# Performance work log

Hardware: AMD Instinct MI355X
Metric: run time of the kernel (lower is better)

## Reference

```python
import jax, jax.numpy as jnp
import numpy as np

EPS = 1e-12

def _l2norm(v, axis):
    n = jnp.sqrt(jnp.sum(v * v, axis=axis, keepdims=True))
    return v / jnp.maximum(n, EPS)

def setup_inputs() -> dict:
    key = jax.random.key(0)
    k1, k2, k3, k4 = jax.random.split(key, 4)
    N, T, D, K = 8, 2048, 512, 64
    x = jax.random.normal(k1, (N, T, D), dtype=jnp.float32)
    W = jax.random.normal(k2, (K, D), dtype=jnp.float32) * (1.0 / np.sqrt(D))  # Conv1d(k=1) weight squeezed
    b = jax.random.normal(k3, (K,), dtype=jnp.float32) * 0.01
    centroids = jax.random.uniform(k4, (K, D), dtype=jnp.float32)
    return {"x": x, "W": W, "b": b, "centroids": centroids}

def reference(x, W, b, centroids):
    N, T, D = x.shape
    K = centroids.shape[0]
    # L2-normalize descriptors along feature dim
    xn = _l2norm(x, axis=2)                                  # [N,T,D]
    # Conv1d with kernel_size=1 == per-timestep linear: [N,K,T] logits over clusters
    logits = jnp.einsum('ntd,kd->nkt', xn, W) + b[None, :, None]
    a = jax.nn.softmax(logits, axis=1)                       # soft assignment over K
    # Algebraically equal to sum_t a[n,k,t] * (xn[n,t,:] - c[k,:])
    vlad = jnp.einsum('nkt,ntd->nkd', a, xn) \
         - jnp.sum(a, axis=2)[:, :, None] * centroids[None]  # [N,K,D]
    vlad = _l2norm(vlad, axis=2)                             # intra-normalize per cluster
    vlad = vlad.reshape(N, K * D)
    return _l2norm(vlad, axis=1)                             # global L2 normalize
```

## Files before the change

### kernel.cpp

```cpp
#include <hip/hip_runtime.h>
#include <math.h>

#define EPS 1e-12f
#define NN 8
#define TT 2048
#define DD 512
#define KK 64

typedef short short8 __attribute__((ext_vector_type(8)));
typedef float floatx4 __attribute__((ext_vector_type(4)));

__device__ __forceinline__ unsigned short f2bf(float f) {
    unsigned int u = __float_as_uint(f);
    u += 0x7FFFu + ((u >> 16) & 1u);
    return (unsigned short)(u >> 16);
}
__device__ __forceinline__ unsigned int pack2(float a, float b) {
    return (unsigned int)f2bf(a) | ((unsigned int)f2bf(b) << 16);
}


__global__ __launch_bounds__(256) void k0_prep(const float* __restrict__ W,
                                               unsigned short* __restrict__ Wb,
                                               float* __restrict__ asum) {
    int i = blockIdx.x * 256 + threadIdx.x;
    Wb[i] = f2bf(W[i]);
    if (i < NN * KK) asum[i] = 0.0f;
}

__global__ __launch_bounds__(256) void kA(const float* __restrict__ x,
                                          const unsigned short* __restrict__ Wb,
                                          const float* __restrict__ bias,
                                          unsigned short* __restrict__ xb,
                                          unsigned short* __restrict__ aTs,
                                          float* __restrict__ asum) {
    const int tid = threadIdx.x;
    const int w = tid >> 6, lane = tid & 63;
    const int l = lane & 15, q = lane >> 4;
    const int row0 = blockIdx.x * 64 + w * 16;
    const int row = row0 + l;
    const int n = row0 >> 11;
    const int tl0 = row0 & (TT - 1);

    const float* xr = x + (size_t)row * DD;
    unsigned short* xo = xb + (size_t)row * DD;
    short8 fragA[16];
    float ssq = 0.0f;
#pragma unroll
    for (int s = 0; s < 16; ++s) {
        float4 u0 = *(const float4*)(xr + s * 32 + q * 8);
        float4 u1 = *(const float4*)(xr + s * 32 + q * 8 + 4);
        ssq += u0.x*u0.x + u0.y*u0.y + u0.z*u0.z + u0.w*u0.w
             + u1.x*u1.x + u1.y*u1.y + u1.z*u1.z + u1.w*u1.w;
        uint4 pk;
        pk.x = pack2(u0.x, u0.y); pk.y = pack2(u0.z, u0.w);
        pk.z = pack2(u1.x, u1.y); pk.w = pack2(u1.z, u1.w);
        union { uint4 u; short8 s8; } cvt; cvt.u = pk;
        fragA[s] = cvt.s8;
        *(uint4*)(xo + s * 32 + q * 8) = pk;
    }
    ssq += __shfl_xor(ssq, 16, 64);
    ssq += __shfl_xor(ssq, 32, 64);
    float st = 1.0f / fmaxf(sqrtf(ssq), EPS);

    floatx4 acc[4];
#pragma unroll
    for (int h = 0; h < 4; ++h) acc[h] = floatx4{0.f, 0.f, 0.f, 0.f};
#pragma unroll
    for (int s = 0; s < 16; ++s) {
#pragma unroll
        for (int h = 0; h < 4; ++h) {
            short8 wf = *(const short8*)(Wb + (size_t)(h * 16 + l) * DD + s * 32 + q * 8);
            acc[h] = __builtin_amdgcn_mfma_f32_16x16x32_bf16(fragA[s], wf, acc[h], 0, 0, 0);
        }
    }

    float sr[4];
#pragma unroll
    for (int r = 0; r < 4; ++r) sr[r] = __shfl(st, 4 * q + r, 64);
    float bj[4];
#pragma unroll
    for (int h = 0; h < 4; ++h) bj[h] = bias[h * 16 + l];

    float av[4][4];
#pragma unroll
    for (int r = 0; r < 4; ++r) {
        float v0 = acc[0][r] * sr[r] + bj[0], v1 = acc[1][r] * sr[r] + bj[1];
        float v2 = acc[2][r] * sr[r] + bj[2], v3 = acc[3][r] * sr[r] + bj[3];
        float m = fmaxf(fmaxf(v0, v1), fmaxf(v2, v3));
#pragma unroll
        for (int msk = 1; msk <= 8; msk <<= 1) m = fmaxf(m, __shfl_xor(m, msk, 64));
        float e0 = __expf(v0 - m), e1 = __expf(v1 - m), e2 = __expf(v2 - m), e3 = __expf(v3 - m);
        float ssum = e0 + e1 + e2 + e3;
#pragma unroll
        for (int msk = 1; msk <= 8; msk <<= 1) ssum += __shfl_xor(ssum, msk, 64);
        float inv = 1.0f / ssum;
        av[0][r] = e0 * inv; av[1][r] = e1 * inv; av[2][r] = e2 * inv; av[3][r] = e3 * inv;
    }

#pragma unroll
    for (int h = 0; h < 4; ++h) {
        uint2 p;
        p.x = pack2(av[h][0] * sr[0], av[h][1] * sr[1]);
        p.y = pack2(av[h][2] * sr[2], av[h][3] * sr[3]);
        *(uint2*)(aTs + ((size_t)(n * KK + h * 16 + l)) * TT + tl0 + 4 * q) = p;
    }
#pragma unroll
    for (int h = 0; h < 4; ++h) {
        float sh = av[h][0] + av[h][1] + av[h][2] + av[h][3];
        sh += __shfl_xor(sh, 16, 64);
        sh += __shfl_xor(sh, 32, 64);
        if (q == 0) atomicAdd(&asum[n * KK + h * 16 + l], sh);
    }
}

__global__ __launch_bounds__(256) void kB(const unsigned short* __restrict__ xb,
                                          const unsigned short* __restrict__ aTs,
                                          float* __restrict__ part) {
    __shared__ unsigned char smem[17408];
    unsigned short* sX0 = (unsigned short*)smem;
    unsigned short* sX1 = sX0 + 4096;
    float* sT = (float*)smem;

    const int tid = threadIdx.x;
    const int wv = tid >> 6, lane = tid & 63;
    const int l = lane & 15, q = lane >> 4;
    const int bid = blockIdx.x;
    const int tc = bid & 7, dt = (bid >> 3) & 7, n = bid >> 6;

    const int ts = tid & 63, dq = tid >> 6;
    const unsigned short* xbase = xb + ((size_t)(n * TT + tc * 256)) * DD + dt * 64 + dq * 16;
    const int g = ts >> 3, t7 = ts & 7;

#define STAGE(S, BUF)                                                          \
    {                                                                          \
        const unsigned short* p_ = xbase + (size_t)((S) * 64 + ts) * DD;       \
        unsigned short vals[16];                                               \
        *(uint4*)(vals) = *(const uint4*)(p_);                                 \
        *(uint4*)(vals + 8) = *(const uint4*)(p_ + 8);                         \
        _Pragma("unroll")                                                      \
        for (int e = 0; e < 16; ++e) {                                         \
            int d_ = dq * 16 + e;                                              \
            (BUF)[d_ * 64 + ((g ^ (d_ & 7)) << 3) + t7] = vals[e];             \
        }                                                                      \
    }

    floatx4 acc[4];
#pragma unroll
    for (int nt = 0; nt < 4; ++nt) acc[nt] = floatx4{0.f, 0.f, 0.f, 0.f};
    const unsigned short* abase = aTs + ((size_t)(n * KK + wv * 16 + l)) * TT + tc * 256;

    STAGE(0, sX0);
    __syncthreads();
#pragma unroll
    for (int s = 0; s < 4; ++s) {
        unsigned short* cur = (s & 1) ? sX1 : sX0;
        unsigned short* nxt = (s & 1) ? sX0 : sX1;
        if (s < 3) {
            if (s == 0) STAGE(1, nxt)
            else if (s == 1) STAGE(2, nxt)
            else STAGE(3, nxt)
        }
#pragma unroll
        for (int kb = 0; kb < 2; ++kb) {
            short8 af = *(const short8*)(abase + s * 64 + kb * 32 + q * 8);
            int gg = q + 4 * kb;
#pragma unroll
            for (int nt = 0; nt < 4; ++nt) {
                int d = nt * 16 + l;
                short8 bf = *(const short8*)(cur + d * 64 + ((gg ^ (d & 7)) << 3));
                acc[nt] = __builtin_amdgcn_mfma_f32_16x16x32_bf16(af, bf, acc[nt], 0, 0, 0);
            }
        }
        __syncthreads();
    }
#undef STAGE

#pragma unroll
    for (int nt = 0; nt < 4; ++nt)
#pragma unroll
        for (int r = 0; r < 4; ++r)
            sT[(wv * 16 + 4 * q + r) * 68 + nt * 16 + l] = acc[nt][r];
    __syncthreads();

    float* pbase = part + ((size_t)(tc * 512 + n * KK)) * DD + dt * 64;
    const int fq = tid & 15, kr = tid >> 4;
#pragma unroll
    for (int i = 0; i < 4; ++i) {
        int k = i * 16 + kr;
        float4 val = *(float4*)(sT + k * 68 + fq * 4);
        *(float4*)(pbase + (size_t)k * DD + fq * 4) = val;
    }
}

__global__ __launch_bounds__(128) void kC(const float* __restrict__ part,
                                          const float* __restrict__ asum,
                                          const float* __restrict__ cent,
                                          float* __restrict__ v,
                                          float* __restrict__ norms) {
    __shared__ float red[2];
    const int nk = blockIdx.x;
    const int k = nk & 63;
    const int tid = threadIdx.x;
    float as = asum[nk];
    float4 cc = ((const float4*)(cent + (size_t)k * DD))[tid];
    float4 a4 = make_float4(-as * cc.x, -as * cc.y, -as * cc.z, -as * cc.w);
#pragma unroll
    for (int tc = 0; tc < 8; ++tc) {
        float4 p = ((const float4*)(part + ((size_t)(tc * 512 + nk)) * DD))[tid];
        a4.x += p.x; a4.y += p.y; a4.z += p.z; a4.w += p.w;
    }
    ((float4*)(v + (size_t)nk * DD))[tid] = a4;
    float ssq = a4.x*a4.x + a4.y*a4.y + a4.z*a4.z + a4.w*a4.w;
#pragma unroll
    for (int m = 32; m >= 1; m >>= 1) ssq += __shfl_xor(ssq, m, 64);
    if ((tid & 63) == 0) red[tid >> 6] = ssq;
    __syncthreads();
    if (tid == 0) norms[nk] = red[0] + red[1];
}

__global__ __launch_bounds__(256) void kD(const float* __restrict__ v,
                                          const float* __restrict__ norms,
                                          float* __restrict__ out) {
    const int n = blockIdx.x >> 3, kg = blockIdx.x & 7;
    const int tid = threadIdx.x;
    float g2 = 0.0f;
#pragma unroll
    for (int k = 0; k < 64; ++k) {
        float nr = sqrtf(norms[n * KK + k]);
        float t = nr / fmaxf(nr, EPS);
        g2 += t * t;
    }
    float g = sqrtf(g2);
    int k = kg * 8 + (tid >> 5);
    float nr = sqrtf(norms[n * KK + k]);
    float s = 1.0f / (fmaxf(nr, EPS) * fmaxf(g, EPS));
    const float4* vp = (const float4*)(v + ((size_t)(n * KK + k)) * DD) + (tid & 31) * 4;
    float4* op = (float4*)(out + ((size_t)(n * KK + k)) * DD) + (tid & 31) * 4;
#pragma unroll
    for (int i = 0; i < 4; ++i) {
        float4 t4 = vp[i];
        t4.x *= s; t4.y *= s; t4.z *= s; t4.w *= s;
        op[i] = t4;
    }
}

extern "C" void kernel_launch(void* const* d_in, const int* in_sizes, int n_in,
                              void* d_out, int out_size, void* d_ws, size_t ws_size,
                              hipStream_t stream) {
    const float* x    = (const float*)d_in[0];
    const float* W    = (const float*)d_in[1];
    const float* b    = (const float*)d_in[2];
    const float* cent = (const float*)d_in[3];
    float* out = (float*)d_out;

    float* w = (float*)d_ws;
    unsigned short* Wb  = (unsigned short*)(w + 0);
    unsigned short* xb  = (unsigned short*)(w + 16384);
    unsigned short* aTs = (unsigned short*)(w + 4210688);
    float* part  = w + 4734976;
    float* v     = w + 6832128;
    float* asum  = w + 7094272;
    float* norms = w + 7094784;

    hipLaunchKernelGGL(k0_prep, dim3(128), dim3(256), 0, stream, W, Wb, asum);
    hipLaunchKernelGGL(kA,      dim3(256), dim3(256), 0, stream, x, Wb, b, xb, aTs, asum);
    hipLaunchKernelGGL(kB,      dim3(512), dim3(256), 0, stream, xb, aTs, part);
    hipLaunchKernelGGL(kC,      dim3(512), dim3(128), 0, stream, part, asum, cent, v, norms);
    hipLaunchKernelGGL(kD,      dim3(64),  dim3(256), 0, stream, v, norms, out);
}
```

Before: 108.5 us.

## Fuse weight prep and final normalization, replace asum atomics with partials

Drops the separate W-to-bf16 prep kernel: each kA block converts W into a 64KB LDS tile laid out in MFMA fragment order. The asum atomics become per-block partial sums that kC reduces. kD is folded into kC, because after intra-normalization every cluster row has unit norm, so the global norm is the constant 8. It also remaps kB block indices. This cuts two launches and the intermediate v/norms traffic, but each kA block now re-reads all of W and uses a large LDS footprint.

```diff
diff --git a/kernel.cpp b/kernel.cpp
--- a/kernel.cpp
+++ b/kernel.cpp
@@ -20,21 +20,17 @@
 }
 
 
-__global__ __launch_bounds__(256) void k0_prep(const float* __restrict__ W,
-                                               unsigned short* __restrict__ Wb,
-                                               float* __restrict__ asum) {
-    int i = blockIdx.x * 256 + threadIdx.x;
-    Wb[i] = f2bf(W[i]);
-    if (i < NN * KK) asum[i] = 0.0f;
-}
-
 __global__ __launch_bounds__(256) void kA(const float* __restrict__ x,
-                                          const unsigned short* __restrict__ Wb,
+                                          const float* __restrict__ W,
                                           const float* __restrict__ bias,
                                           unsigned short* __restrict__ xb,
                                           unsigned short* __restrict__ aTs,
-                                          float* __restrict__ asum) {
+                                          float* __restrict__ asumP) {
+    __shared__ unsigned short sW[32768];
+    __shared__ float sRed[256];
+
     const int tid = threadIdx.x;
+
     const int w = tid >> 6, lane = tid & 63;
     const int l = lane & 15, q = lane >> 4;
     const int row0 = blockIdx.x * 64 + w * 16;
@@ -59,10 +55,28 @@
         fragA[s] = cvt.s8;
         *(uint4*)(xo + s * 32 + q * 8) = pk;
     }
+
+    {
+        const int sp = tid >> 4, hp = (tid >> 2) & 3, qp = tid & 3;
+        const float* wsrc = W + (size_t)(hp * 16) * DD + sp * 32 + qp * 8;
+        unsigned short* wdst = sW + (size_t)tid * 128;
+#pragma unroll
+        for (int j = 0; j < 16; ++j) {
+            float4 u0 = *(const float4*)(wsrc + (size_t)j * DD);
+            float4 u1 = *(const float4*)(wsrc + (size_t)j * DD + 4);
+            uint4 pk;
+            pk.x = pack2(u0.x, u0.y); pk.y = pack2(u0.z, u0.w);
+            pk.z = pack2(u1.x, u1.y); pk.w = pack2(u1.z, u1.w);
+            *(uint4*)(wdst + j * 8) = pk;
+        }
+    }
+
     ssq += __shfl_xor(ssq, 16, 64);
     ssq += __shfl_xor(ssq, 32, 64);
     float st = 1.0f / fmaxf(sqrtf(ssq), EPS);
 
+    __syncthreads();
+
     floatx4 acc[4];
 #pragma unroll
     for (int h = 0; h < 4; ++h) acc[h] = floatx4{0.f, 0.f, 0.f, 0.f};
@@ -70,7 +84,7 @@
     for (int s = 0; s < 16; ++s) {
 #pragma unroll
         for (int h = 0; h < 4; ++h) {
-            short8 wf = *(const short8*)(Wb + (size_t)(h * 16 + l) * DD + s * 32 + q * 8);
+            short8 wf = *(const short8*)(sW + ((size_t)((s * 4 + h) * 64) + lane) * 8);
             acc[h] = __builtin_amdgcn_mfma_f32_16x16x32_bf16(fragA[s], wf, acc[h], 0, 0, 0);
         }
     }
@@ -91,10 +105,10 @@
 #pragma unroll
         for (int msk = 1; msk <= 8; msk <<= 1) m = fmaxf(m, __shfl_xor(m, msk, 64));
         float e0 = __expf(v0 - m), e1 = __expf(v1 - m), e2 = __expf(v2 - m), e3 = __expf(v3 - m);
-        float ssum = e0 + e1 + e2 + e3;
-#pragma unroll
-        for (int msk = 1; msk <= 8; msk <<= 1) ssum += __shfl_xor(ssum, msk, 64);
-        float inv = 1.0f / ssum;
+        float ss = e0 + e1 + e2 + e3;
+#pragma unroll
+        for (int msk = 1; msk <= 8; msk <<= 1) ss += __shfl_xor(ss, msk, 64);
+        float inv = 1.0f / ss;
         av[0][r] = e0 * inv; av[1][r] = e1 * inv; av[2][r] = e2 * inv; av[3][r] = e3 * inv;
     }
 
@@ -105,12 +119,18 @@
         p.y = pack2(av[h][2] * sr[2], av[h][3] * sr[3]);
         *(uint2*)(aTs + ((size_t)(n * KK + h * 16 + l)) * TT + tl0 + 4 * q) = p;
     }
+
 #pragma unroll
     for (int h = 0; h < 4; ++h) {
         float sh = av[h][0] + av[h][1] + av[h][2] + av[h][3];
         sh += __shfl_xor(sh, 16, 64);
         sh += __shfl_xor(sh, 32, 64);
-        if (q == 0) atomicAdd(&asum[n * KK + h * 16 + l], sh);
+        if (q == 0) sRed[w * 64 + h * 16 + l] = sh;
+    }
+    __syncthreads();
+    if (tid < 64) {
+        float s0 = sRed[tid] + sRed[64 + tid] + sRed[128 + tid] + sRed[192 + tid];
+        asumP[(size_t)blockIdx.x * 64 + tid] = s0;
     }
 }
 
@@ -126,7 +146,8 @@
     const int wv = tid >> 6, lane = tid & 63;
     const int l = lane & 15, q = lane >> 4;
     const int bid = blockIdx.x;
-    const int tc = bid & 7, dt = (bid >> 3) & 7, n = bid >> 6;
+    const int low = bid & 63;
+    const int n = low >> 3, tc = low & 7, dt = bid >> 6;
 
     const int ts = tid & 63, dq = tid >> 6;
     const unsigned short* xbase = xb + ((size_t)(n * TT + tc * 256)) * DD + dt * 64 + dq * 16;
@@ -194,15 +215,24 @@
 }
 
 __global__ __launch_bounds__(128) void kC(const float* __restrict__ part,
-                                          const float* __restrict__ asum,
+                                          const float* __restrict__ asumP,
                                           const float* __restrict__ cent,
-                                          float* __restrict__ v,
-                                          float* __restrict__ norms) {
+                                          float* __restrict__ out) {
     __shared__ float red[2];
+    __shared__ float sAsum;
     const int nk = blockIdx.x;
-    const int k = nk & 63;
+    const int n = nk >> 6, k = nk & 63;
     const int tid = threadIdx.x;
-    float as = asum[nk];
+
+    if (tid < 32) {
+        float p = asumP[(size_t)(n * 32 + tid) * 64 + k];
+#pragma unroll
+        for (int m = 16; m >= 1; m >>= 1) p += __shfl_xor(p, m, 64);
+        if (tid == 0) sAsum = p;
+    }
+    __syncthreads();
+    float as = sAsum;
+
     float4 cc = ((const float4*)(cent + (size_t)k * DD))[tid];
     float4 a4 = make_float4(-as * cc.x, -as * cc.y, -as * cc.z, -as * cc.w);
 #pragma unroll
@@ -210,39 +240,15 @@
         float4 p = ((const float4*)(part + ((size_t)(tc * 512 + nk)) * DD))[tid];
         a4.x += p.x; a4.y += p.y; a4.z += p.z; a4.w += p.w;
     }
-    ((float4*)(v + (size_t)nk * DD))[tid] = a4;
     float ssq = a4.x*a4.x + a4.y*a4.y + a4.z*a4.z + a4.w*a4.w;
 #pragma unroll
     for (int m = 32; m >= 1; m >>= 1) ssq += __shfl_xor(ssq, m, 64);
     if ((tid & 63) == 0) red[tid >> 6] = ssq;
     __syncthreads();
-    if (tid == 0) norms[nk] = red[0] + red[1];
-}
-
-__global__ __launch_bounds__(256) void kD(const float* __restrict__ v,
-                                          const float* __restrict__ norms,
-                                          float* __restrict__ out) {
-    const int n = blockIdx.x >> 3, kg = blockIdx.x & 7;
-    const int tid = threadIdx.x;
-    float g2 = 0.0f;
-#pragma unroll
-    for (int k = 0; k < 64; ++k) {
-        float nr = sqrtf(norms[n * KK + k]);
-        float t = nr / fmaxf(nr, EPS);
-        g2 += t * t;
-    }
-    float g = sqrtf(g2);
-    int k = kg * 8 + (tid >> 5);
-    float nr = sqrtf(norms[n * KK + k]);
-    float s = 1.0f / (fmaxf(nr, EPS) * fmaxf(g, EPS));
-    const float4* vp = (const float4*)(v + ((size_t)(n * KK + k)) * DD) + (tid & 31) * 4;
-    float4* op = (float4*)(out + ((size_t)(n * KK + k)) * DD) + (tid & 31) * 4;
-#pragma unroll
-    for (int i = 0; i < 4; ++i) {
-        float4 t4 = vp[i];
-        t4.x *= s; t4.y *= s; t4.z *= s; t4.w *= s;
-        op[i] = t4;
-    }
+    float nr = sqrtf(red[0] + red[1]);
+    float sc = 1.0f / (fmaxf(nr, EPS) * 8.0f);
+    a4.x *= sc; a4.y *= sc; a4.z *= sc; a4.w *= sc;
+    ((float4*)(out + (size_t)nk * DD))[tid] = a4;
 }
 
 extern "C" void kernel_launch(void* const* d_in, const int* in_sizes, int n_in,
@@ -255,17 +261,12 @@
     float* out = (float*)d_out;
 
     float* w = (float*)d_ws;
-    unsigned short* Wb  = (unsigned short*)(w + 0);
-    unsigned short* xb  = (unsigned short*)(w + 16384);
-    unsigned short* aTs = (unsigned short*)(w + 4210688);
-    float* part  = w + 4734976;
-    float* v     = w + 6832128;
-    float* asum  = w + 7094272;
-    float* norms = w + 7094784;
-
-    hipLaunchKernelGGL(k0_prep, dim3(128), dim3(256), 0, stream, W, Wb, asum);
-    hipLaunchKernelGGL(kA,      dim3(256), dim3(256), 0, stream, x, Wb, b, xb, aTs, asum);
-    hipLaunchKernelGGL(kB,      dim3(512), dim3(256), 0, stream, xb, aTs, part);
-    hipLaunchKernelGGL(kC,      dim3(512), dim3(128), 0, stream, part, asum, cent, v, norms);
-    hipLaunchKernelGGL(kD,      dim3(64),  dim3(256), 0, stream, v, norms, out);
-}
+    unsigned short* xb  = (unsigned short*)(w + 0);
+    unsigned short* aTs = (unsigned short*)(w + 4194304);
+    float* part  = w + 4718592;
+    float* asumP = w + 6815744;
+
+    hipLaunchKernelGGL(kA, dim3(256), dim3(256), 0, stream, x, W, b, xb, aTs, asumP);
+    hipLaunchKernelGGL(kB, dim3(512), dim3(256), 0, stream, xb, aTs, part);
+    hipLaunchKernelGGL(kC, dim3(512), dim3(128), 0, stream, part, asumP, cent, out);
+}
```

Result: faster. 96.47 us (-11.1%).
